# Kernel tuning notes

Measured on AMD Instinct MI355X. Metric: run time of the kernel, lower is better.

The kernel has to match this reference:

```python
import jax, jax.numpy as jnp
import numpy as np

N_TOK = 2048      # flattened batch*seq tokens
D_MODEL = 1024    # in_features
D_INT = 512       # d_intermediate
N_EXPERTS = 8     # n_routed_experts
TOP_K = 2         # n_activated_experts


def setup_inputs() -> dict:
    key = jax.random.key(0)
    k1, k2, k3, k4, k5 = jax.random.split(key, 5)
    x = jax.random.normal(k1, (N_TOK, D_MODEL), dtype=jnp.float32)
    indices = jax.random.randint(k2, (N_TOK, TOP_K), 0, N_EXPERTS, dtype=jnp.int32)
    # router combine weights (normalized over top-k like a softmax router)
    weights = jax.nn.softmax(jax.random.normal(k3, (N_TOK, TOP_K), dtype=jnp.float32), axis=-1)
    # tokens-per-expert counts, consistent with indices (as the router would supply)
    counts = jnp.bincount(indices.reshape(-1), length=N_EXPERTS).astype(jnp.int32)
    # expert weights: fc1 -> 2*d_int (gated MLP), fc2 -> d_model; kaiming-ish scale
    s1 = 1.0 / np.sqrt(D_MODEL)
    s2 = 1.0 / np.sqrt(D_INT)
    fc1_weight = jax.random.uniform(k4, (N_EXPERTS, 2 * D_INT, D_MODEL), jnp.float32, -s1, s1)
    fc2_weight = jax.random.uniform(k5, (N_EXPERTS, D_MODEL, D_INT), jnp.float32, -s2, s2)
    return {"x": x, "weights": weights, "indices": indices, "counts": counts,
            "fc1_weight": fc1_weight, "fc2_weight": fc2_weight}


def reference(x, weights, indices, counts, fc1_weight, fc2_weight):
    # Dense dispatch-free formulation: run every token through every expert's
    # gated MLP, then gather the per-slot expert output. Identical math to the
    # sort / grouped-GEMM / scatter path for the selected (token, expert) pairs.
    # h: (n_tok, n_experts, 2*d_int)
    h = jnp.einsum('td,egd->teg', x, fc1_weight)
    y, z = jnp.split(h, 2, axis=-1)
    a = y * jax.nn.silu(z)  # GatedMLP: y * activation(z)
    # expert outputs: (n_tok, n_experts, d_model)
    out = jnp.einsum('tei,edi->ted', a, fc2_weight)
    # gather the chosen expert output for each of the top-k slots: (n_tok, k, d_model)
    per_slot = jnp.take_along_axis(out, indices[:, :, None], axis=1)
    # combine: z = bmm(weights[:, None], x_by_expert).squeeze(1)
    return jnp.einsum('tk,tkd->td', weights, per_slot)
```

## Files before the change

kernel.cpp:

```cpp
#include <hip/hip_runtime.h>

typedef unsigned short u16;
typedef unsigned int u32;
using short8  = __attribute__((ext_vector_type(8))) short;
using floatx4 = __attribute__((ext_vector_type(4))) float;

#define N_TOK   2048
#define D_MODEL 1024
#define D_INT   512
#define NE      8

#define O_TOK    0
#define O_WROW   24576
#define O_XG     65536
#define O_ACT    10551296
#define O_FC1B   36765696
#define O_FC2B   53542912

static __device__ inline u16 f2bf(float f) {
    u32 u = __builtin_bit_cast(u32, f);
    u = (u + 0x7fffu + ((u >> 16) & 1u)) >> 16;
    return (u16)u;
}
static __device__ inline u32 pack2(float a, float b) {
    return (u32)f2bf(a) | ((u32)f2bf(b) << 16);
}
static __device__ inline void glds16(const u16* g, u16* l) {
    __builtin_amdgcn_global_load_lds(
        (const __attribute__((address_space(1))) void*)g,
        (__attribute__((address_space(3))) void*)l, 16, 0, 0);
}

__global__ __launch_bounds__(256) void prep_kernel(
    const float* __restrict__ x, const float* __restrict__ wts,
    const int* __restrict__ indices, const int* __restrict__ counts,
    const float* __restrict__ fc1, const float* __restrict__ fc2,
    u16* __restrict__ fc1b, u16* __restrict__ fc2b,
    u16* __restrict__ Xg, int* __restrict__ tok, float* __restrict__ wrow,
    float* __restrict__ out) {
    int b = blockIdx.x, tid = threadIdx.x;
    if (b < 6144) {
        size_t v = (size_t)b * 256 + tid;
        const float* src; u16* dst; size_t off;
        if (v < 1048576) { src = fc1; dst = fc1b; off = v * 8; }
        else             { src = fc2; dst = fc2b; off = (v - 1048576) * 8; }
        const floatx4* s4 = reinterpret_cast<const floatx4*>(src + off);
        floatx4 a = s4[0], bb = s4[1];
        uint4 o;
        o.x = pack2(a[0], a[1]); o.y = pack2(a[2], a[3]);
        o.z = pack2(bb[0], bb[1]); o.w = pack2(bb[2], bb[3]);
        *reinterpret_cast<uint4*>(dst + off) = o;
        return;
    }
    if (b < 8192) {
        int t = b - 6144;
        int off[NE];
        {
            int acc = 0;
            #pragma unroll
            for (int e = 0; e < NE; e++) { off[e] = acc; acc += ((counts[e] + 63) >> 6) << 6; }
        }
        int e0 = indices[2 * t], e1 = indices[2 * t + 1];
        __shared__ int s0, s1;
        if (tid == 0) { s0 = 0; s1 = 0; }
        __syncthreads();
        int c0 = 0, c1 = 0;
        const int4* ip = reinterpret_cast<const int4*>(indices);
        #pragma unroll
        for (int i = 0; i < 4; i++) {
            int4 vv = ip[tid * 4 + i];
            int q = tid * 16 + i * 4;
            c0 += (q + 0 < 2 * t && vv.x == e0) + (q + 1 < 2 * t && vv.y == e0)
                + (q + 2 < 2 * t && vv.z == e0) + (q + 3 < 2 * t && vv.w == e0);
            c1 += (q + 0 <= 2 * t && vv.x == e1) + (q + 1 <= 2 * t && vv.y == e1)
                + (q + 2 <= 2 * t && vv.z == e1) + (q + 3 <= 2 * t && vv.w == e1);
        }
        if (c0) atomicAdd(&s0, c0);
        if (c1) atomicAdd(&s1, c1);
        __syncthreads();
        int r0 = off[e0] + s0;
        int r1 = off[e1] + s1;
        if (tid == 0) {
            tok[r0] = t; tok[r1] = t;
            wrow[r0] = wts[2 * t]; wrow[r1] = wts[2 * t + 1];
        }
        const floatx4* src = reinterpret_cast<const floatx4*>(x + (size_t)t * D_MODEL);
        floatx4 a = src[tid];
        uint2 o;
        o.x = pack2(a[0], a[1]); o.y = pack2(a[2], a[3]);
        *reinterpret_cast<uint2*>(Xg + (size_t)r0 * D_MODEL + tid * 4) = o;
        *reinterpret_cast<uint2*>(Xg + (size_t)r1 * D_MODEL + tid * 4) = o;
        return;
    }
    {
        int z = b - 8192;
        floatx4* dst = reinterpret_cast<floatx4*>(out) + (size_t)z * 1024;
        #pragma unroll
        for (int i = 0; i < 4; i++) dst[i * 256 + tid] = (floatx4){0.f, 0.f, 0.f, 0.f};
        return;
    }
}

static __device__ inline int xcd_swz576(int bid) {
    return (bid & 7) * 72 + (bid >> 3);
}

__global__ __launch_bounds__(256) void gemm1_kernel(
    const u16* __restrict__ Xg, const u16* __restrict__ fc1b,
    u16* __restrict__ Act, const int* __restrict__ counts) {
    __shared__ u16 As[64 * 64];
    __shared__ u16 Bs[128 * 64];
    int tid = threadIdx.x;
    int soff[NE + 1];
    {
        int acc = 0;
        #pragma unroll
        for (int e2 = 0; e2 < NE; e2++) { soff[e2] = acc; acc += ((counts[e2] + 63) >> 6) << 6; }
        soff[NE] = acc;
    }
    int t = xcd_swz576(blockIdx.x);
    int bx = t & 7, by = t >> 3;
    int row0 = by * 64;
    if (row0 >= soff[NE]) return;
    int e = 0;
    while (soff[e + 1] <= row0) e++;
    const u16* A  = Xg + (size_t)row0 * 1024;
    const u16* Be = fc1b + (size_t)e * 1024 * 1024;

    int lane = tid & 63, w = tid >> 6;
    int m0 = (w >> 1) * 32, n0 = (w & 1) * 32;
    int lr = lane & 15, kq = lane >> 4;

    const u16* gA[2]; u16* lA[2];
    #pragma unroll
    for (int j = 0; j < 2; j++) {
        int v = tid + j * 256;
        int r = v >> 3, kb = (v & 7) ^ (r & 7);
        gA[j] = A + (size_t)r * 1024 + kb * 8;
        lA[j] = As + (w * 64 + j * 256) * 8;
    }
    const u16* gB[4]; u16* lB[4];
    #pragma unroll
    for (int j = 0; j < 4; j++) {
        int v = tid + j * 256;
        int r = v >> 3, kb = (v & 7) ^ (r & 7);
        int grow = (r < 64) ? (bx * 64 + r) : (448 + bx * 64 + r);
        gB[j] = Be + (size_t)grow * 1024 + kb * 8;
        lB[j] = Bs + (w * 64 + j * 256) * 8;
    }

    floatx4 aY[2][2], aZ[2][2];
    #pragma unroll
    for (int i = 0; i < 2; i++)
        #pragma unroll
        for (int j = 0; j < 2; j++) {
            aY[i][j] = (floatx4){0.f, 0.f, 0.f, 0.f};
            aZ[i][j] = (floatx4){0.f, 0.f, 0.f, 0.f};
        }

    for (int k0 = 0; k0 < 1024; k0 += 64) {
        glds16(gA[0] + k0, lA[0]); glds16(gA[1] + k0, lA[1]);
        glds16(gB[0] + k0, lB[0]); glds16(gB[1] + k0, lB[1]);
        glds16(gB[2] + k0, lB[2]); glds16(gB[3] + k0, lB[3]);
        __syncthreads();
        #pragma unroll
        for (int ks = 0; ks < 2; ks++) {
            int sw = ((ks * 4 + kq) ^ (lr & 7)) * 8;
            short8 af[2], by2[2], bz[2];
            #pragma unroll
            for (int i = 0; i < 2; i++)
                af[i] = *reinterpret_cast<const short8*>(&As[(m0 + i * 16 + lr) * 64 + sw]);
            #pragma unroll
            for (int j = 0; j < 2; j++) {
                by2[j] = *reinterpret_cast<const short8*>(&Bs[(n0 + j * 16 + lr) * 64 + sw]);
                bz[j]  = *reinterpret_cast<const short8*>(&Bs[(64 + n0 + j * 16 + lr) * 64 + sw]);
            }
            #pragma unroll
            for (int i = 0; i < 2; i++)
                #pragma unroll
                for (int j = 0; j < 2; j++) {
                    aY[i][j] = __builtin_amdgcn_mfma_f32_16x16x32_bf16(af[i], by2[j], aY[i][j], 0, 0, 0);
                    aZ[i][j] = __builtin_amdgcn_mfma_f32_16x16x32_bf16(af[i], bz[j], aZ[i][j], 0, 0, 0);
                }
        }
        __syncthreads();
    }
    #pragma unroll
    for (int i = 0; i < 2; i++)
        #pragma unroll
        for (int j = 0; j < 2; j++) {
            floatx4 y = aY[i][j], z = aZ[i][j];
            #pragma unroll
            for (int r = 0; r < 4; r++) {
                float zz = z[r];
                float av = y[r] * (zz / (1.0f + __expf(-zz)));
                int m = m0 + i * 16 + kq * 4 + r;
                int g = bx * 64 + n0 + j * 16 + lr;
                Act[(size_t)(row0 + m) * D_INT + g] = f2bf(av);
            }
        }
}

__global__ __launch_bounds__(256) void gemm2_kernel(
    const u16* __restrict__ Act, const u16* __restrict__ fc2b,
    float* __restrict__ out, const int* __restrict__ counts,
    const int* __restrict__ tok, const float* __restrict__ wrow) {
    __shared__ u16 As[64 * 64];
    __shared__ u16 Bs[128 * 64];
    __shared__ int sTok[64];
    __shared__ float sW[64];
    int tid = threadIdx.x;
    int soff[NE + 1];
    {
        int acc = 0;
        #pragma unroll
        for (int e2 = 0; e2 < NE; e2++) { soff[e2] = acc; acc += ((counts[e2] + 63) >> 6) << 6; }
        soff[NE] = acc;
    }
    int t = xcd_swz576(blockIdx.x);
    int bx = t & 7, by = t >> 3;
    int row0 = by * 64;
    if (row0 >= soff[NE]) return;
    int e = 0;
    while (soff[e + 1] <= row0) e++;
    const u16* A  = Act + (size_t)row0 * 512;
    const u16* Be = fc2b + (size_t)e * 1024 * 512;

    int lane = tid & 63, w = tid >> 6;
    int m0 = (w >> 1) * 32, n0 = (w & 1) * 64;
    int lr = lane & 15, kq = lane >> 4;

    const u16* gA[2]; u16* lA[2];
    #pragma unroll
    for (int j = 0; j < 2; j++) {
        int v = tid + j * 256;
        int r = v >> 3, kb = (v & 7) ^ (r & 7);
        gA[j] = A + (size_t)r * 512 + kb * 8;
        lA[j] = As + (w * 64 + j * 256) * 8;
    }
    const u16* gB[4]; u16* lB[4];
    #pragma unroll
    for (int j = 0; j < 4; j++) {
        int v = tid + j * 256;
        int r = v >> 3, kb = (v & 7) ^ (r & 7);
        gB[j] = Be + (size_t)(bx * 128 + r) * 512 + kb * 8;
        lB[j] = Bs + (w * 64 + j * 256) * 8;
    }

    floatx4 acc[2][4];
    #pragma unroll
    for (int i = 0; i < 2; i++)
        #pragma unroll
        for (int j = 0; j < 4; j++) acc[i][j] = (floatx4){0.f, 0.f, 0.f, 0.f};

    for (int k0 = 0; k0 < 512; k0 += 64) {
        glds16(gA[0] + k0, lA[0]); glds16(gA[1] + k0, lA[1]);
        glds16(gB[0] + k0, lB[0]); glds16(gB[1] + k0, lB[1]);
        glds16(gB[2] + k0, lB[2]); glds16(gB[3] + k0, lB[3]);
        __syncthreads();
        #pragma unroll
        for (int ks = 0; ks < 2; ks++) {
            int sw = ((ks * 4 + kq) ^ (lr & 7)) * 8;
            short8 af[2], bf[4];
            #pragma unroll
            for (int i = 0; i < 2; i++)
                af[i] = *reinterpret_cast<const short8*>(&As[(m0 + i * 16 + lr) * 64 + sw]);
            #pragma unroll
            for (int j = 0; j < 4; j++)
                bf[j] = *reinterpret_cast<const short8*>(&Bs[(n0 + j * 16 + lr) * 64 + sw]);
            #pragma unroll
            for (int i = 0; i < 2; i++)
                #pragma unroll
                for (int j = 0; j < 4; j++)
                    acc[i][j] = __builtin_amdgcn_mfma_f32_16x16x32_bf16(af[i], bf[j], acc[i][j], 0, 0, 0);
        }
        __syncthreads();
    }
    if (tid < 64) {
        int g = row0 + tid;
        bool val = (g - soff[e]) < counts[e];
        sTok[tid] = val ? tok[g] : -1;
        sW[tid]   = val ? wrow[g] : 0.f;
    }
    __syncthreads();
    #pragma unroll
    for (int i = 0; i < 2; i++)
        #pragma unroll
        for (int r = 0; r < 4; r++) {
            int m = m0 + i * 16 + kq * 4 + r;
            int tk = sTok[m];
            if (tk >= 0) {
                float wgt = sW[m];
                float* dst = out + (size_t)tk * D_MODEL + bx * 128;
                #pragma unroll
                for (int j = 0; j < 4; j++)
                    atomicAdd(dst + n0 + j * 16 + lr, wgt * acc[i][j][r]);
            }
        }
}

extern "C" void kernel_launch(void* const* d_in, const int* in_sizes, int n_in,
                              void* d_out, int out_size, void* d_ws, size_t ws_size,
                              hipStream_t stream) {
    const float* x       = (const float*)d_in[0];
    const float* wts     = (const float*)d_in[1];
    const int*   indices = (const int*)d_in[2];
    const int*   counts  = (const int*)d_in[3];
    const float* fc1     = (const float*)d_in[4];
    const float* fc2     = (const float*)d_in[5];
    float* out = (float*)d_out;
    char* ws = (char*)d_ws;

    int*   tok  = (int*)(ws + O_TOK);
    float* wrow = (float*)(ws + O_WROW);
    u16*   Xg   = (u16*)(ws + O_XG);
    u16*   Act  = (u16*)(ws + O_ACT);
    u16*   fc1b = (u16*)(ws + O_FC1B);
    u16*   fc2b = (u16*)(ws + O_FC2B);

    prep_kernel<<<8704, 256, 0, stream>>>(x, wts, indices, counts, fc1, fc2,
                                          fc1b, fc2b, Xg, tok, wrow, out);
    gemm1_kernel<<<576, 256, 0, stream>>>(Xg, fc1b, Act, counts);
    gemm2_kernel<<<576, 256, 0, stream>>>(Act, fc2b, out, counts, tok, wrow);
}
```

Baseline: 148.7 us.

## Move fc2 conversion and output zeroing into gemm1 grid to overlap with GEMM

The fc2 fp32-to-bf16 conversion and the zeroing of the output buffer move out of the prep kernel and into extra blocks appended to the gemm1 launch. Those blocks run beside the GEMM tiles, so their memory traffic can overlap gemm1 compute instead of lengthening the serial prep phase. The risk is that the extra blocks compete with GEMM blocks for bandwidth and CU slots, and their scheduling order relative to the GEMM tiles is not controlled.

```diff
diff --git a/kernel.cpp b/kernel.cpp
--- a/kernel.cpp
+++ b/kernel.cpp
@@ -34,26 +34,22 @@
 __global__ __launch_bounds__(256) void prep_kernel(
     const float* __restrict__ x, const float* __restrict__ wts,
     const int* __restrict__ indices, const int* __restrict__ counts,
-    const float* __restrict__ fc1, const float* __restrict__ fc2,
-    u16* __restrict__ fc1b, u16* __restrict__ fc2b,
-    u16* __restrict__ Xg, int* __restrict__ tok, float* __restrict__ wrow,
-    float* __restrict__ out) {
+    const float* __restrict__ fc1, u16* __restrict__ fc1b,
+    u16* __restrict__ Xg, int* __restrict__ tok, float* __restrict__ wrow) {
     int b = blockIdx.x, tid = threadIdx.x;
-    if (b < 6144) {
+    if (b < 4096) {
         size_t v = (size_t)b * 256 + tid;
-        const float* src; u16* dst; size_t off;
-        if (v < 1048576) { src = fc1; dst = fc1b; off = v * 8; }
-        else             { src = fc2; dst = fc2b; off = (v - 1048576) * 8; }
-        const floatx4* s4 = reinterpret_cast<const floatx4*>(src + off);
+        size_t off = v * 8;
+        const floatx4* s4 = reinterpret_cast<const floatx4*>(fc1 + off);
         floatx4 a = s4[0], bb = s4[1];
         uint4 o;
         o.x = pack2(a[0], a[1]); o.y = pack2(a[2], a[3]);
         o.z = pack2(bb[0], bb[1]); o.w = pack2(bb[2], bb[3]);
-        *reinterpret_cast<uint4*>(dst + off) = o;
+        *reinterpret_cast<uint4*>(fc1b + off) = o;
         return;
     }
-    if (b < 8192) {
-        int t = b - 6144;
+    {
+        int t = b - 4096;
         int off[NE];
         {
             int acc = 0;
@@ -92,13 +88,6 @@
         *reinterpret_cast<uint2*>(Xg + (size_t)r1 * D_MODEL + tid * 4) = o;
         return;
     }
-    {
-        int z = b - 8192;
-        floatx4* dst = reinterpret_cast<floatx4*>(out) + (size_t)z * 1024;
-        #pragma unroll
-        for (int i = 0; i < 4; i++) dst[i * 256 + tid] = (floatx4){0.f, 0.f, 0.f, 0.f};
-        return;
-    }
 }
 
 static __device__ inline int xcd_swz576(int bid) {
@@ -107,10 +96,31 @@
 
 __global__ __launch_bounds__(256) void gemm1_kernel(
     const u16* __restrict__ Xg, const u16* __restrict__ fc1b,
-    u16* __restrict__ Act, const int* __restrict__ counts) {
+    u16* __restrict__ Act, const int* __restrict__ counts,
+    const float* __restrict__ fc2, u16* __restrict__ fc2b,
+    float* __restrict__ out) {
     __shared__ u16 As[64 * 64];
     __shared__ u16 Bs[128 * 64];
     int tid = threadIdx.x;
+    int b = blockIdx.x;
+    if (b >= 576) {
+        if (b < 2624) {
+            size_t v = (size_t)(b - 576) * 256 + tid;
+            size_t off = v * 8;
+            const floatx4* s4 = reinterpret_cast<const floatx4*>(fc2 + off);
+            floatx4 a = s4[0], bb = s4[1];
+            uint4 o;
+            o.x = pack2(a[0], a[1]); o.y = pack2(a[2], a[3]);
+            o.z = pack2(bb[0], bb[1]); o.w = pack2(bb[2], bb[3]);
+            *reinterpret_cast<uint4*>(fc2b + off) = o;
+        } else {
+            int z = b - 2624;
+            floatx4* dst = reinterpret_cast<floatx4*>(out) + (size_t)z * 1024;
+            #pragma unroll
+            for (int i = 0; i < 4; i++) dst[i * 256 + tid] = (floatx4){0.f, 0.f, 0.f, 0.f};
+        }
+        return;
+    }
     int soff[NE + 1];
     {
         int acc = 0;
@@ -118,7 +128,7 @@
         for (int e2 = 0; e2 < NE; e2++) { soff[e2] = acc; acc += ((counts[e2] + 63) >> 6) << 6; }
         soff[NE] = acc;
     }
-    int t = xcd_swz576(blockIdx.x);
+    int t = xcd_swz576(b);
     int bx = t & 7, by = t >> 3;
     int row0 = by * 64;
     if (row0 >= soff[NE]) return;
@@ -318,8 +328,8 @@
     u16*   fc1b = (u16*)(ws + O_FC1B);
     u16*   fc2b = (u16*)(ws + O_FC2B);
 
-    prep_kernel<<<8704, 256, 0, stream>>>(x, wts, indices, counts, fc1, fc2,
-                                          fc1b, fc2b, Xg, tok, wrow, out);
-    gemm1_kernel<<<576, 256, 0, stream>>>(Xg, fc1b, Act, counts);
+    prep_kernel<<<6144, 256, 0, stream>>>(x, wts, indices, counts, fc1, fc1b,
+                                          Xg, tok, wrow);
+    gemm1_kernel<<<3136, 256, 0, stream>>>(Xg, fc1b, Act, counts, fc2, fc2b, out);
     gemm2_kernel<<<576, 256, 0, stream>>>(Act, fc2b, out, counts, tok, wrow);
 }
```

Result: no change. 147.2 us (-1.0%).
